# Performance work log

Measured on AMD Instinct MI355X. Metric: run time of the kernel, lower is better.

Reference implementation:

```python
import jax, jax.numpy as jnp
import numpy as np

DIM_CAP = 16   # capsule dim
NCLS = 17      # annotation_nr
BS = 16
T = 120        # chunk_size * fps
P = 22         # players per frame graph
G = BS * T     # number of graphs = 1920
N = G * P      # nodes = 42240
C_IN = 14
CHS = [16, 32, 64, 152]  # 8m,16m,32m,76m with m=2
BN_EPS = 1e-3


def _build_graph():
    # fully-connected directed edges within each 22-node graph (no self loops)
    ii, jj = np.meshgrid(np.arange(P), np.arange(P), indexing='ij')
    mask = ii != jj
    li, lj = ii[mask], jj[mask]               # (462,)
    base = (np.arange(G) * P)[:, None]
    src = (base + li[None, :]).reshape(-1)
    dst = (base + lj[None, :]).reshape(-1)
    edge_index = np.stack([src, dst]).astype(np.int64)   # (2, E)
    batch = np.repeat(np.arange(G), P).astype(np.int64)  # (N,)
    return jnp.asarray(edge_index), jnp.asarray(batch)


def setup_inputs() -> dict:
    key = jax.random.key(0)
    ks = jax.random.split(key, 16)
    edge_index, batch = _build_graph()
    E = edge_index.shape[1]
    x = jax.random.normal(ks[0], (N, C_IN), dtype=jnp.float32)
    edge_attr = jax.random.uniform(ks[1], (E, 5), dtype=jnp.float32)
    dims = [C_IN] + CHS
    params = {}
    for i in range(4):
        s = 1.0 / np.sqrt(dims[i])
        params[f'W{i+1}'] = jax.random.normal(ks[2 + i], (dims[i], dims[i + 1]), dtype=jnp.float32) * s
        params[f'b{i+1}'] = jnp.zeros((dims[i + 1],), dtype=jnp.float32)
    c_out = DIM_CAP * NCLS  # 272
    params['conv_w'] = jax.random.normal(ks[6], (c_out, CHS[-1], 3), dtype=jnp.float32) * (1.0 / np.sqrt(CHS[-1] * 3))
    params['conv_b'] = jnp.zeros((c_out,), dtype=jnp.float32)
    params['bn_gamma'] = jnp.ones((T,), dtype=jnp.float32)
    params['bn_beta'] = jnp.zeros((T,), dtype=jnp.float32)
    return dict(x=x, edge_index=edge_index, batch=batch, edge_attr=edge_attr, **params)


def _gcn_layer(x, src, dst, w_edge, W, b):
    # PyG GCNConv: x' = D^-1/2 (A + I) D^-1/2 (x W) + b, edge weights w, self-loop weight 1
    n = x.shape[0]
    h = x @ W
    loop = jnp.arange(n)
    src_f = jnp.concatenate([src, loop])
    dst_f = jnp.concatenate([dst, loop])
    w_f = jnp.concatenate([w_edge, jnp.ones((n,), h.dtype)])
    deg = jax.ops.segment_sum(w_f, dst_f, num_segments=n)
    dinv = jnp.where(deg > 0, jax.lax.rsqrt(deg), 0.0)
    norm = dinv[src_f] * w_f * dinv[dst_f]
    out = jax.ops.segment_sum(norm[:, None] * h[src_f], dst_f, num_segments=n)
    return out + b


def reference(x, edge_index, batch, edge_attr, W1, b1, W2, b2, W3, b3, W4, b4,
              conv_w, conv_b, bn_gamma, bn_beta):
    src, dst = edge_index[0], edge_index[1]
    ew = edge_attr[:, 4]
    h = jax.nn.relu(_gcn_layer(x, src, dst, ew, W1, b1))
    h = jax.nn.relu(_gcn_layer(h, src, dst, ew, W2, b2))
    h = jax.nn.relu(_gcn_layer(h, src, dst, ew, W3, b3))
    h = jax.nn.relu(_gcn_layer(h, src, dst, ew, W4, b4))
    # global mean pool per graph -> (G, 152)
    ones = jnp.ones((h.shape[0],), h.dtype)
    cnt = jax.ops.segment_sum(ones, batch, num_segments=G)
    pooled = jax.ops.segment_sum(h, batch, num_segments=G) / jnp.clip(cnt, 1.0)[:, None]
    # (BS, T, 152) -> (BS, 152, T); conv kernel (3,1) with pad (1,1) on T
    feat = pooled.reshape(BS, T, CHS[-1]).transpose(0, 2, 1)
    conv = jax.lax.conv_general_dilated(
        feat, conv_w, window_strides=(1,), padding=[(1, 1)],
        dimension_numbers=('NCH', 'OIH', 'NCH'))
    conv = conv + conv_b[None, :, None]            # (BS, 272, T)
    caps = conv.transpose(0, 2, 1).reshape(BS, T, DIM_CAP, NCLS)
    # BatchNorm2d(num_features=T) in eval mode: running mean 0, var 1
    scale = (bn_gamma / jnp.sqrt(1.0 + BN_EPS))[None, :, None, None]
    shift = bn_beta[None, :, None, None]
    s = jax.nn.sigmoid(caps * scale + shift)
    out = jnp.sqrt(jnp.sum(jnp.square(s - 0.5), axis=2) * 4.0 / DIM_CAP)
    return out  # (BS, T, NCLS)
```

## Files before the change

kernel.cpp:

```cpp
#include <hip/hip_runtime.h>
#include <hip/hip_bf16.h>

#define GROUPS 1920
#define CH4 152

__device__ __forceinline__ int rh(int r) { return (r + (r >> 3)) & 7; }
__device__ __forceinline__ int swz(int r, int c) {
    return (r << 5) + ((((c >> 2) ^ rh(r)) << 2) | (c & 3));
}
__device__ __forceinline__ int swz4(int r, int c4) {
    return (r << 5) + ((c4 ^ rh(r)) << 2);
}

template<int DIN, int KR>
__device__ __forceinline__ void layerA(const float* buf, float* Ut,
                                       const float* A, int tid)
{
    constexpr int NT = (DIN / KR) * 3;
    if (tid < NT) {
        const int kt = tid / 3, pt = tid - kt * 3;
        const int p0 = pt * 8;
        float acc[KR][8];
        #pragma unroll
        for (int j = 0; j < KR; ++j)
            #pragma unroll
            for (int a = 0; a < 8; ++a) acc[j][a] = 0.f;
        #pragma unroll 2
        for (int q = 0; q < 22; ++q) {
            const float4 a0 = *(const float4*)(A + q * 28 + p0);
            const float4 a1 = *(const float4*)(A + q * 28 + p0 + 4);
            float xv[KR];
            #pragma unroll
            for (int j = 0; j < KR; ++j) xv[j] = buf[swz(kt * KR + j, q)];
            #pragma unroll
            for (int j = 0; j < KR; ++j) {
                acc[j][0] = fmaf(xv[j], a0.x, acc[j][0]);
                acc[j][1] = fmaf(xv[j], a0.y, acc[j][1]);
                acc[j][2] = fmaf(xv[j], a0.z, acc[j][2]);
                acc[j][3] = fmaf(xv[j], a0.w, acc[j][3]);
                acc[j][4] = fmaf(xv[j], a1.x, acc[j][4]);
                acc[j][5] = fmaf(xv[j], a1.y, acc[j][5]);
                acc[j][6] = fmaf(xv[j], a1.z, acc[j][6]);
                acc[j][7] = fmaf(xv[j], a1.w, acc[j][7]);
            }
        }
        #pragma unroll
        for (int j = 0; j < KR; ++j) {
            const int k = kt * KR + j;
            *(float4*)(Ut + swz4(k, pt * 2)) =
                make_float4(acc[j][0], acc[j][1], acc[j][2], acc[j][3]);
            *(float4*)(Ut + swz4(k, pt * 2 + 1)) =
                make_float4(acc[j][4], acc[j][5], acc[j][6], acc[j][7]);
        }
    }
}

template<int DIN, int DOUT, int CR>
__device__ __forceinline__ void layerB(const float* __restrict__ W,
                                       const float* __restrict__ Bb,
                                       const float* Ut, float* buf, int tid)
{
    constexpr int NT = (DOUT / CR) * 3;
    if (tid < NT) {
        const int ct = tid / 3, pt = tid - ct * 3;
        const int c0 = ct * CR;
        float acc[CR][8];
        #pragma unroll
        for (int b = 0; b < CR; ++b) {
            const float bias = Bb[c0 + b];
            #pragma unroll
            for (int a = 0; a < 8; ++a) acc[b][a] = bias;
        }
        #pragma unroll 4
        for (int k = 0; k < DIN; ++k) {
            const float4 u0 = *(const float4*)(Ut + swz4(k, pt * 2));
            const float4 u1 = *(const float4*)(Ut + swz4(k, pt * 2 + 1));
            float wv[CR];
            if constexpr (CR == 1) {
                wv[0] = W[k * DOUT + c0];
            } else if constexpr (CR == 2) {
                const float2 w2 = *(const float2*)(W + k * DOUT + c0);
                wv[0] = w2.x; wv[1] = w2.y;
            } else {
                #pragma unroll
                for (int b = 0; b < CR; b += 4) {
                    const float4 w4 = *(const float4*)(W + k * DOUT + c0 + b);
                    wv[b] = w4.x; wv[b + 1] = w4.y; wv[b + 2] = w4.z; wv[b + 3] = w4.w;
                }
            }
            #pragma unroll
            for (int b = 0; b < CR; ++b) {
                acc[b][0] = fmaf(wv[b], u0.x, acc[b][0]);
                acc[b][1] = fmaf(wv[b], u0.y, acc[b][1]);
                acc[b][2] = fmaf(wv[b], u0.z, acc[b][2]);
                acc[b][3] = fmaf(wv[b], u0.w, acc[b][3]);
                acc[b][4] = fmaf(wv[b], u1.x, acc[b][4]);
                acc[b][5] = fmaf(wv[b], u1.y, acc[b][5]);
                acc[b][6] = fmaf(wv[b], u1.z, acc[b][6]);
                acc[b][7] = fmaf(wv[b], u1.w, acc[b][7]);
            }
        }
        #pragma unroll
        for (int b = 0; b < CR; ++b) {
            const int r = c0 + b;
            *(float4*)(buf + swz4(r, pt * 2)) =
                make_float4(fmaxf(acc[b][0], 0.f), fmaxf(acc[b][1], 0.f),
                            fmaxf(acc[b][2], 0.f), fmaxf(acc[b][3], 0.f));
            *(float4*)(buf + swz4(r, pt * 2 + 1)) =
                make_float4(fmaxf(acc[b][4], 0.f), fmaxf(acc[b][5], 0.f),
                            fmaxf(acc[b][6], 0.f), fmaxf(acc[b][7], 0.f));
        }
    }
}

__global__ __launch_bounds__(128, 4) void gcn_kernel(
    const float* __restrict__ x, const float* __restrict__ ea,
    const float* __restrict__ W1, const float* __restrict__ b1,
    const float* __restrict__ W2, const float* __restrict__ b2,
    const float* __restrict__ W3, const float* __restrict__ b3,
    const float* __restrict__ W4, const float* __restrict__ b4,
    float* __restrict__ pooled)
{
    __shared__ __align__(16) float sA[24 * 28];
    __shared__ float dv[24];
    __shared__ __align__(16) float buf[64 * 32];
    __shared__ __align__(16) float Ut[64 * 32];

    const int tid = threadIdx.x;
    const int g = blockIdx.x;

    for (int idx = tid; idx < 24 * 28; idx += 128) {
        const int q = idx / 28, p = idx - q * 28;
        float v = 0.f;
        if (q < 22 && p < 22) {
            if (q == p) v = 1.0f;
            else {
                const int e = q * 21 + p - (p > q);
                v = ea[((size_t)g * 462 + e) * 5 + 4];
            }
        }
        sA[idx] = v;
    }
    for (int idx = tid; idx < 14 * 24; idx += 128) {
        const int k = idx / 24, p = idx - k * 24;
        buf[swz(k, p)] = (p < 22) ? x[((size_t)g * 22 + p) * 14 + k] : 0.f;
    }
    __syncthreads();

    if (tid < 24) {
        const int p = tid;
        float s = 0.f;
        #pragma unroll
        for (int q = 0; q < 22; ++q) s += sA[q * 28 + p];
        dv[p] = (s > 0.f) ? rsqrtf(s) : 0.f;
    }
    __syncthreads();
    for (int idx = tid; idx < 24 * 28; idx += 128) {
        const int q = idx / 28, p = idx - q * 28;
        if (p < 24) sA[idx] *= dv[q] * dv[p];
    }
    __syncthreads();

    layerA<14, 1>(buf, Ut, sA, tid);           __syncthreads();
    layerB<14, 16, 1>(W1, b1, Ut, buf, tid);   __syncthreads();
    layerA<16, 1>(buf, Ut, sA, tid);           __syncthreads();
    layerB<16, 32, 1>(W2, b2, Ut, buf, tid);   __syncthreads();
    layerA<32, 1>(buf, Ut, sA, tid);           __syncthreads();
    layerB<32, 64, 2>(W3, b3, Ut, buf, tid);   __syncthreads();
    layerA<64, 2>(buf, Ut, sA, tid);           __syncthreads();

    float* pscr = sA;
    if (tid < 38 * 3) {
        const int ct = tid / 3, pt = tid - ct * 3;
        const int c0 = ct * 4;
        float acc[4][8];
        #pragma unroll
        for (int b = 0; b < 4; ++b) {
            const float bias = b4[c0 + b];
            #pragma unroll
            for (int a = 0; a < 8; ++a) acc[b][a] = bias;
        }
        #pragma unroll 4
        for (int k = 0; k < 64; ++k) {
            const float4 u0 = *(const float4*)(Ut + swz4(k, pt * 2));
            const float4 u1 = *(const float4*)(Ut + swz4(k, pt * 2 + 1));
            const float4 w4 = *(const float4*)(W4 + k * 152 + c0);
            const float wv[4] = {w4.x, w4.y, w4.z, w4.w};
            #pragma unroll
            for (int b = 0; b < 4; ++b) {
                acc[b][0] = fmaf(wv[b], u0.x, acc[b][0]);
                acc[b][1] = fmaf(wv[b], u0.y, acc[b][1]);
                acc[b][2] = fmaf(wv[b], u0.z, acc[b][2]);
                acc[b][3] = fmaf(wv[b], u0.w, acc[b][3]);
                acc[b][4] = fmaf(wv[b], u1.x, acc[b][4]);
                acc[b][5] = fmaf(wv[b], u1.y, acc[b][5]);
                acc[b][6] = fmaf(wv[b], u1.z, acc[b][6]);
                acc[b][7] = fmaf(wv[b], u1.w, acc[b][7]);
            }
        }
        const int alim = (pt == 2) ? 6 : 8;
        float ps[4];
        #pragma unroll
        for (int b = 0; b < 4; ++b) {
            float s = 0.f;
            #pragma unroll
            for (int a = 0; a < 8; ++a)
                s += (a < alim) ? fmaxf(acc[b][a], 0.f) : 0.f;
            ps[b] = s;
        }
        *(float4*)(pscr + pt * 152 + c0) = make_float4(ps[0], ps[1], ps[2], ps[3]);
    }
    __syncthreads();

    {
        const int b = g / 120, t = g - b * 120;
        float* dst = pooled + ((size_t)(b * 122) + t + 1) * 152;
        for (int c = tid; c < 152; c += 128) {
            const float s = pscr[c] + pscr[152 + c] + pscr[304 + c];
            dst[c] = s * (1.0f / 22.0f);
        }
    }
}

__global__ __launch_bounds__(256) void repack_conv_w(const float* __restrict__ cw,
                                                     float* __restrict__ wT,
                                                     float* __restrict__ pG)
{
    const int idx = blockIdx.x * 256 + threadIdx.x;
    if (idx < 272 * 456) {
        const int o = idx / 456, r = idx - o * 456;
        wT[r * 272 + o] = cw[idx];
    } else {
        const int j = idx - 272 * 456;
        if (j < 16 * 2 * 152) {
            const int bb = j / 304, rr = j - bb * 304;
            const int row = (rr < 152) ? 0 : 121;
            const int c = (rr < 152) ? rr : rr - 152;
            pG[((size_t)bb * 122 + row) * 152 + c] = 0.f;
        }
    }
}

__global__ __launch_bounds__(320) void conv_caps_kernel(
    const float* __restrict__ pG, const float* __restrict__ wT,
    const float* __restrict__ cb, const float* __restrict__ gamma,
    const float* __restrict__ beta, float* __restrict__ out)
{
    __shared__ __align__(16) float s2[8 * 272];
    __shared__ float sc[8], sh[8];

    const int bx = blockIdx.x;
    const int b = bx / 15, tile = bx - b * 15;
    const int t0 = tile * 8;
    const int tid = threadIdx.x;

    if (tid < 8) {
        const int t = t0 + tid;
        sc[tid] = gamma[t] * 0.999500374688f;
        sh[tid] = beta[t];
    }
    __syncthreads();

    if (tid < 272) {
        const int o = tid;
        const float cb0 = cb[o];
        float acc[8];
        #pragma unroll
        for (int tt = 0; tt < 8; ++tt) acc[tt] = cb0;
        const float* wp0 = wT + o;
        const float* frow0 = pG + ((size_t)b * 122 + t0) * 152;
        float w0 = wp0[0], w1 = wp0[272], w2 = wp0[544];
        #pragma unroll 2
        for (int i = 0; i < CH4; ++i) {
            const int inext = (i == CH4 - 1) ? i : i + 1;
            const float* nwp = wp0 + inext * 816;
            const float nw0 = nwp[0], nw1 = nwp[272], nw2 = nwp[544];
            const float* f = frow0 + i;
            float fr[10];
            #pragma unroll
            for (int j = 0; j < 10; ++j) fr[j] = f[j * 152];
            #pragma unroll
            for (int tt = 0; tt < 8; ++tt)
                acc[tt] = fmaf(w0, fr[tt], fmaf(w1, fr[tt + 1], fmaf(w2, fr[tt + 2], acc[tt])));
            w0 = nw0; w1 = nw1; w2 = nw2;
        }
        #pragma unroll
        for (int tt = 0; tt < 8; ++tt) {
            const float z = fmaf(acc[tt], sc[tt], sh[tt]);
            const float s = 1.0f / (1.0f + __expf(-z));
            const float d = s - 0.5f;
            s2[tt * 272 + o] = d * d;
        }
    }
    __syncthreads();

    for (int e = tid; e < 8 * 17; e += 320) {
        const int tt = e / 17, n = e - tt * 17;
        float s = 0.f;
        #pragma unroll
        for (int d = 0; d < 16; ++d) s += s2[tt * 272 + d * 17 + n];
        out[((size_t)b * 120 + t0 + tt) * 17 + n] = sqrtf(s) * 0.5f;
    }
}

extern "C" void kernel_launch(void* const* d_in, const int* in_sizes, int n_in,
                              void* d_out, int out_size, void* d_ws, size_t ws_size,
                              hipStream_t stream) {
    const float* x     = (const float*)d_in[0];
    const float* ea    = (const float*)d_in[3];
    const float* W1    = (const float*)d_in[4];
    const float* b1    = (const float*)d_in[5];
    const float* W2    = (const float*)d_in[6];
    const float* b2    = (const float*)d_in[7];
    const float* W3    = (const float*)d_in[8];
    const float* b3    = (const float*)d_in[9];
    const float* W4    = (const float*)d_in[10];
    const float* b4    = (const float*)d_in[11];
    const float* cw    = (const float*)d_in[12];
    const float* cb    = (const float*)d_in[13];
    const float* gamma = (const float*)d_in[14];
    const float* beta  = (const float*)d_in[15];
    float* out = (float*)d_out;

    float* pG = (float*)d_ws;
    float* wT = pG + (size_t)16 * 122 * 152;

    hipLaunchKernelGGL(repack_conv_w,
                       dim3((272 * 456 + 16 * 2 * 152 + 255) / 256),
                       dim3(256), 0, stream, cw, wT, pG);
    hipLaunchKernelGGL(gcn_kernel, dim3(GROUPS), dim3(128), 0, stream,
                       x, ea, W1, b1, W2, b2, W3, b3, W4, b4, pG);
    hipLaunchKernelGGL(conv_caps_kernel, dim3(16 * 15), dim3(320), 0, stream,
                       pG, wT, cb, gamma, beta, out);
}
```

Before: 161.0 us.

## Fold weight repack into GCN kernel and split conv over channel halves

Removes the separate repack launch by having each GCN block transpose a slice of the conv weights and zero the padding rows of the pooled buffer. The conv kernel now uses 4-timestep tiles (twice as many blocks) and splits the 152-channel reduction across two 320-thread halves, combining partial sums through shared memory. The aim is to cut one launch and raise parallelism in the tail conv kernel. The cost is more redundant feature loads per output and an extra sync.

Measured after the change: 173.7 us. +7.9%, slower.

```diff
diff --git a/kernel.cpp b/kernel.cpp
--- a/kernel.cpp
+++ b/kernel.cpp
@@ -1,5 +1,4 @@
 #include <hip/hip_runtime.h>
-#include <hip/hip_bf16.h>
 
 #define GROUPS 1920
 #define CH4 152
@@ -119,6 +118,7 @@
     const float* __restrict__ W2, const float* __restrict__ b2,
     const float* __restrict__ W3, const float* __restrict__ b3,
     const float* __restrict__ W4, const float* __restrict__ b4,
+    const float* __restrict__ cw, float* __restrict__ wT,
     float* __restrict__ pooled)
 {
     __shared__ __align__(16) float sA[24 * 28];
@@ -128,6 +128,17 @@
 
     const int tid = threadIdx.x;
     const int g = blockIdx.x;
+    const int b = g / 120, t = g - b * 120;
+
+    {
+        const int idx = g * 128 + tid;
+        if (idx < 272 * 456) {
+            const int o = idx / 456, r = idx - o * 456;
+            wT[r * 272 + o] = cw[idx];
+        }
+    }
+    if (t == 0 && tid < 152)   pooled[((size_t)(b * 122) + 0)   * 152 + tid] = 0.f;
+    if (t == 119 && tid < 152) pooled[((size_t)(b * 122) + 121) * 152 + tid] = 0.f;
 
     for (int idx = tid; idx < 24 * 28; idx += 128) {
         const int q = idx / 28, p = idx - q * 28;
@@ -175,10 +186,10 @@
         const int c0 = ct * 4;
         float acc[4][8];
         #pragma unroll
-        for (int b = 0; b < 4; ++b) {
-            const float bias = b4[c0 + b];
-            #pragma unroll
-            for (int a = 0; a < 8; ++a) acc[b][a] = bias;
+        for (int bb = 0; bb < 4; ++bb) {
+            const float bias = b4[c0 + bb];
+            #pragma unroll
+            for (int a = 0; a < 8; ++a) acc[bb][a] = bias;
         }
         #pragma unroll 4
         for (int k = 0; k < 64; ++k) {
@@ -187,33 +198,32 @@
             const float4 w4 = *(const float4*)(W4 + k * 152 + c0);
             const float wv[4] = {w4.x, w4.y, w4.z, w4.w};
             #pragma unroll
-            for (int b = 0; b < 4; ++b) {
-                acc[b][0] = fmaf(wv[b], u0.x, acc[b][0]);
-                acc[b][1] = fmaf(wv[b], u0.y, acc[b][1]);
-                acc[b][2] = fmaf(wv[b], u0.z, acc[b][2]);
-                acc[b][3] = fmaf(wv[b], u0.w, acc[b][3]);
-                acc[b][4] = fmaf(wv[b], u1.x, acc[b][4]);
-                acc[b][5] = fmaf(wv[b], u1.y, acc[b][5]);
-                acc[b][6] = fmaf(wv[b], u1.z, acc[b][6]);
-                acc[b][7] = fmaf(wv[b], u1.w, acc[b][7]);
+            for (int bb = 0; bb < 4; ++bb) {
+                acc[bb][0] = fmaf(wv[bb], u0.x, acc[bb][0]);
+                acc[bb][1] = fmaf(wv[bb], u0.y, acc[bb][1]);
+                acc[bb][2] = fmaf(wv[bb], u0.z, acc[bb][2]);
+                acc[bb][3] = fmaf(wv[bb], u0.w, acc[bb][3]);
+                acc[bb][4] = fmaf(wv[bb], u1.x, acc[bb][4]);
+                acc[bb][5] = fmaf(wv[bb], u1.y, acc[bb][5]);
+                acc[bb][6] = fmaf(wv[bb], u1.z, acc[bb][6]);
+                acc[bb][7] = fmaf(wv[bb], u1.w, acc[bb][7]);
             }
         }
         const int alim = (pt == 2) ? 6 : 8;
         float ps[4];
         #pragma unroll
-        for (int b = 0; b < 4; ++b) {
+        for (int bb = 0; bb < 4; ++bb) {
             float s = 0.f;
             #pragma unroll
             for (int a = 0; a < 8; ++a)
-                s += (a < alim) ? fmaxf(acc[b][a], 0.f) : 0.f;
-            ps[b] = s;
+                s += (a < alim) ? fmaxf(acc[bb][a], 0.f) : 0.f;
+            ps[bb] = s;
         }
         *(float4*)(pscr + pt * 152 + c0) = make_float4(ps[0], ps[1], ps[2], ps[3]);
     }
     __syncthreads();
 
     {
-        const int b = g / 120, t = g - b * 120;
         float* dst = pooled + ((size_t)(b * 122) + t + 1) * 152;
         for (int c = tid; c < 152; c += 128) {
             const float s = pscr[c] + pscr[152 + c] + pscr[304 + c];
@@ -222,71 +232,54 @@
     }
 }
 
-__global__ __launch_bounds__(256) void repack_conv_w(const float* __restrict__ cw,
-                                                     float* __restrict__ wT,
-                                                     float* __restrict__ pG)
-{
-    const int idx = blockIdx.x * 256 + threadIdx.x;
-    if (idx < 272 * 456) {
-        const int o = idx / 456, r = idx - o * 456;
-        wT[r * 272 + o] = cw[idx];
-    } else {
-        const int j = idx - 272 * 456;
-        if (j < 16 * 2 * 152) {
-            const int bb = j / 304, rr = j - bb * 304;
-            const int row = (rr < 152) ? 0 : 121;
-            const int c = (rr < 152) ? rr : rr - 152;
-            pG[((size_t)bb * 122 + row) * 152 + c] = 0.f;
-        }
-    }
-}
-
-__global__ __launch_bounds__(320) void conv_caps_kernel(
+__global__ __launch_bounds__(640) void conv_caps_kernel(
     const float* __restrict__ pG, const float* __restrict__ wT,
     const float* __restrict__ cb, const float* __restrict__ gamma,
     const float* __restrict__ beta, float* __restrict__ out)
 {
-    __shared__ __align__(16) float s2[8 * 272];
-    __shared__ float sc[8], sh[8];
+    __shared__ __align__(16) float s2[4 * 272];
+    __shared__ float sc[4], sh[4];
 
     const int bx = blockIdx.x;
-    const int b = bx / 15, tile = bx - b * 15;
-    const int t0 = tile * 8;
+    const int b = bx / 30, tile = bx - b * 30;
+    const int t0 = tile * 4;
     const int tid = threadIdx.x;
-
-    if (tid < 8) {
-        const int t = t0 + tid;
-        sc[tid] = gamma[t] * 0.999500374688f;
-        sh[tid] = beta[t];
-    }
-    __syncthreads();
-
-    if (tid < 272) {
-        const int o = tid;
-        const float cb0 = cb[o];
-        float acc[8];
-        #pragma unroll
-        for (int tt = 0; tt < 8; ++tt) acc[tt] = cb0;
-        const float* wp0 = wT + o;
-        const float* frow0 = pG + ((size_t)b * 122 + t0) * 152;
-        float w0 = wp0[0], w1 = wp0[272], w2 = wp0[544];
+    const int half = tid / 320;
+    const int o = tid - half * 320;
+
+    if (tid < 4) {
+        sc[tid] = gamma[t0 + tid] * 0.999500374688f;
+        sh[tid] = beta[t0 + tid];
+    }
+
+    float acc[4];
+    if (o < 272) {
+        const float a0 = half ? 0.f : cb[o];
+        acc[0] = a0; acc[1] = a0; acc[2] = a0; acc[3] = a0;
+        const int i0 = half * 76;
+        const float* wp = wT + (size_t)i0 * 816 + o;
+        const float* f  = pG + ((size_t)b * 122 + t0) * 152 + i0;
         #pragma unroll 2
-        for (int i = 0; i < CH4; ++i) {
-            const int inext = (i == CH4 - 1) ? i : i + 1;
-            const float* nwp = wp0 + inext * 816;
-            const float nw0 = nwp[0], nw1 = nwp[272], nw2 = nwp[544];
-            const float* f = frow0 + i;
-            float fr[10];
-            #pragma unroll
-            for (int j = 0; j < 10; ++j) fr[j] = f[j * 152];
-            #pragma unroll
-            for (int tt = 0; tt < 8; ++tt)
+        for (int i = 0; i < 76; ++i) {
+            const float w0 = wp[0], w1 = wp[272], w2 = wp[544];
+            float fr[6];
+            #pragma unroll
+            for (int j = 0; j < 6; ++j) fr[j] = f[j * 152];
+            #pragma unroll
+            for (int tt = 0; tt < 4; ++tt)
                 acc[tt] = fmaf(w0, fr[tt], fmaf(w1, fr[tt + 1], fmaf(w2, fr[tt + 2], acc[tt])));
-            w0 = nw0; w1 = nw1; w2 = nw2;
-        }
-        #pragma unroll
-        for (int tt = 0; tt < 8; ++tt) {
-            const float z = fmaf(acc[tt], sc[tt], sh[tt]);
+            wp += 816; f += 1;
+        }
+    }
+    if (half == 1 && o < 272) {
+        #pragma unroll
+        for (int tt = 0; tt < 4; ++tt) s2[tt * 272 + o] = acc[tt];
+    }
+    __syncthreads();
+    if (half == 0 && o < 272) {
+        #pragma unroll
+        for (int tt = 0; tt < 4; ++tt) {
+            const float z = fmaf(acc[tt] + s2[tt * 272 + o], sc[tt], sh[tt]);
             const float s = 1.0f / (1.0f + __expf(-z));
             const float d = s - 0.5f;
             s2[tt * 272 + o] = d * d;
@@ -294,8 +287,8 @@
     }
     __syncthreads();
 
-    for (int e = tid; e < 8 * 17; e += 320) {
-        const int tt = e / 17, n = e - tt * 17;
+    if (tid < 4 * 17) {
+        const int tt = tid / 17, n = tid - tt * 17;
         float s = 0.f;
         #pragma unroll
         for (int d = 0; d < 16; ++d) s += s2[tt * 272 + d * 17 + n];
@@ -325,11 +318,8 @@
     float* pG = (float*)d_ws;
     float* wT = pG + (size_t)16 * 122 * 152;
 
-    hipLaunchKernelGGL(repack_conv_w,
-                       dim3((272 * 456 + 16 * 2 * 152 + 255) / 256),
-                       dim3(256), 0, stream, cw, wT, pG);
     hipLaunchKernelGGL(gcn_kernel, dim3(GROUPS), dim3(128), 0, stream,
-                       x, ea, W1, b1, W2, b2, W3, b3, W4, b4, pG);
-    hipLaunchKernelGGL(conv_caps_kernel, dim3(16 * 15), dim3(320), 0, stream,
+                       x, ea, W1, b1, W2, b2, W3, b3, W4, b4, cw, wT, pG);
+    hipLaunchKernelGGL(conv_caps_kernel, dim3(16 * 30), dim3(640), 0, stream,
                        pG, wT, cb, gamma, beta, out);
 }
```
